# Kernel optimization log

Measured on AMD Instinct MI355X. Metric: run time of the kernel, lower is better.

## Reference

```python
import jax, jax.numpy as jnp
import numpy as np

# Pangu-Weather EarthSpecificBlock, layer-1 config
WZ, WH, WW = 2, 6, 12          # window size (z, lat, lon)
Z, H, W = 8, 91, 180           # token grid after patch embedding
C = 192                        # token dim
HEADS = 6
B = 1
PAD_TOP, PAD_BOT = 2, 3        # lat 91 -> 96 (CustomPad3d, centered)
ZP, HP, WP = 8, 96, 180        # padded grid
NWB = (ZP // WZ) * (HP // WH)  # 64 bias windows (z*lat)
N = WZ * WH * WW               # 144 tokens per window


def earth_position_index():
    zi = np.arange(WZ); zj = -np.arange(WZ) * WZ
    hi = np.arange(WH); hj = -np.arange(WH) * WH
    w = np.arange(WW)
    c1 = np.stack(np.meshgrid(zi, hi, w, indexing='ij')).reshape(3, -1)
    c2 = np.stack(np.meshgrid(zj, hj, w, indexing='ij')).reshape(3, -1)
    coords = (c1[:, :, None] - c2[:, None, :]).transpose(1, 2, 0).astype(np.int64)
    coords[:, :, 2] += WW - 1
    coords[:, :, 1] *= 2 * WW - 1
    coords[:, :, 0] *= (2 * WW - 1) * WH * WH
    return coords.sum(-1)  # (N, N) int indices into bias table

POS_IDX = jnp.asarray(earth_position_index())


def layer_norm(x, w, b, eps=1e-5):
    mu = x.mean(-1, keepdims=True)
    var = ((x - mu) ** 2).mean(-1, keepdims=True)
    return (x - mu) * jax.lax.rsqrt(var + eps) * w + b


def setup_inputs() -> dict:
    key = jax.random.key(0)
    ks = jax.random.split(key, 8)
    f = lambda k, s: jax.random.normal(k, s, jnp.float32) * 0.02
    return {
        "x": jax.random.normal(ks[0], (B, Z * H * W, C), jnp.float32),
        "qkv_w": f(ks[1], (3 * C, C)),
        "qkv_b": jnp.zeros((3 * C,), jnp.float32),
        "proj_w": f(ks[2], (C, C)),
        "proj_b": jnp.zeros((C,), jnp.float32),
        "bias_table": f(ks[3], ((2 * WW - 1) * WH * WH * WZ * WZ, NWB, HEADS)),
        "norm1_w": jnp.ones((C,), jnp.float32),
        "norm1_b": jnp.zeros((C,), jnp.float32),
        "norm2_w": jnp.ones((C,), jnp.float32),
        "norm2_b": jnp.zeros((C,), jnp.float32),
        "mlp_w1": f(ks[4], (4 * C, C)),
        "mlp_b1": jnp.zeros((4 * C,), jnp.float32),
        "mlp_w2": f(ks[5], (C, 4 * C)),
        "mlp_b2": jnp.zeros((C,), jnp.float32),
        "roll": 0,
    }


def reference(x, qkv_w, qkv_b, proj_w, proj_b, bias_table,
              norm1_w, norm1_b, norm2_w, norm2_b,
              mlp_w1, mlp_b1, mlp_w2, mlp_b2, roll):
    shortcut = x  # (B, L, C)
    hd = C // HEADS
    scale = hd ** -0.5
    xs = x.reshape(B, Z, H, W, C)
    xs = jnp.pad(xs, ((0, 0), (0, 0), (PAD_TOP, PAD_BOT), (0, 0), (0, 0)))
    # window partition: (B, ZP, HP, WP, C) -> (nb, N, C), windows ordered (z, lat, lon)
    xw = xs.reshape(B, ZP // WZ, WZ, HP // WH, WH, WP // WW, WW, C)
    xw = xw.transpose(0, 1, 3, 5, 2, 4, 6, 7).reshape(-1, N, C)
    nb = xw.shape[0]  # B * 64 * 15 = 960
    qkv = (xw @ qkv_w.T + qkv_b).reshape(nb, N, 3, HEADS, hd).transpose(2, 0, 3, 1, 4)
    q, k, v = qkv[0] * scale, qkv[1], qkv[2]  # each (nb, HEADS, N, hd)
    att = jnp.einsum('bhnd,bhmd->bhnm', q, k)  # (nb, HEADS, N, N)
    # earth-specific bias gathered via position index
    bias = bias_table[POS_IDX]                 # (N, N, NWB, HEADS)
    bias = bias.transpose(2, 3, 0, 1)          # (NWB, HEADS, N, N)
    # nb = B * NWB * n_lon_windows, NWB is the leading window factor
    att = att.reshape(B, NWB, -1, HEADS, N, N) + bias[None, :, None]
    att = jax.nn.softmax(att, axis=-1).reshape(nb, HEADS, N, N)
    out = jnp.einsum('bhnm,bhmd->bnhd', att, v).reshape(nb, N, C)
    out = out @ proj_w.T + proj_b
    # window reverse + crop padding
    out = out.reshape(B, ZP // WZ, HP // WH, WP // WW, WZ, WH, WW, C)
    out = out.transpose(0, 1, 4, 2, 5, 3, 6, 7).reshape(B, ZP, HP, WP, C)
    out = out[:, :, PAD_TOP:HP - PAD_BOT, :, :].reshape(B, -1, C)
    # post-norm residual (Pangu): x = shortcut + norm1(attn); x = x + norm2(mlp(x))
    x1 = shortcut + layer_norm(out, norm1_w, norm1_b)
    h1 = jax.nn.gelu(x1 @ mlp_w1.T + mlp_b1, approximate=False)
    mlp_out = h1 @ mlp_w2.T + mlp_b2
    return x1 + layer_norm(mlp_out, norm2_w, norm2_b)
```

## Files before the change

kernel.cpp:

```cpp
#include <hip/hip_runtime.h>
#include <hip/hip_bf16.h>

typedef __hip_bfloat16 bf16;
#define DEVI __device__ __forceinline__

typedef __bf16 bf16x8 __attribute__((ext_vector_type(8)));
typedef __bf16 bf16x4 __attribute__((ext_vector_type(4)));
typedef float  f32x4  __attribute__((ext_vector_type(4)));

DEVI float bf2f(bf16 v) { return __bfloat162float(v); }
DEVI bf16 f2bf(float v) { return __float2bfloat16(v); }
DEVI float bfu2f(unsigned short u) { return __uint_as_float((unsigned)u << 16); }

DEVI unsigned short bfbits(float x) {
    bf16 h = __float2bfloat16(x);
    return *reinterpret_cast<unsigned short*>(&h);
}
DEVI unsigned int pack2(float x, float y) {
    return (unsigned int)bfbits(x) | ((unsigned int)bfbits(y) << 16);
}
DEVI bf16x8 pack8(float4 lo, float4 hi) {
    union { unsigned int u[4]; bf16x8 v; } z;
    z.u[0] = pack2(lo.x, lo.y); z.u[1] = pack2(lo.z, lo.w);
    z.u[2] = pack2(hi.x, hi.y); z.u[3] = pack2(hi.z, hi.w);
    return z.v;
}
DEVI bf16x8 ld8h(const bf16* p) {
    bf16x4 lo = *(const bf16x4*)p;
    bf16x4 hi = *(const bf16x4*)(p + 4);
    return __builtin_shufflevector(lo, hi, 0, 1, 2, 3, 4, 5, 6, 7);
}

__global__ __launch_bounds__(256) void prep_attn_w(
    const float* __restrict__ qkv_w, const float* __restrict__ qkv_b,
    bf16* __restrict__ qkv_wb, float* __restrict__ qkv_bb)
{
    const float scale = 0.17677669529663687f;
    int idx = blockIdx.x * 256 + threadIdx.x;
    if (idx < 110592) {
        int c = idx % 192, d = idx / 192;
        int h = d / 96, q2 = d - h * 96, seg = q2 >> 5, rr = q2 & 31;
        float v = qkv_w[(size_t)(seg * 192 + h * 32 + rr) * 192 + c];
        if (seg == 0) v *= scale;
        qkv_wb[idx] = f2bf(v);
    }
    if (idx < 576) {
        int h = idx / 96, q2 = idx - h * 96, seg = q2 >> 5, rr = q2 & 31;
        float b = qkv_b[seg * 192 + h * 32 + rr];
        if (seg == 0) b *= scale;
        qkv_bb[idx] = b;
    }
}

__global__ __launch_bounds__(256) void prep_bias(
    const float* __restrict__ bias_table, bf16* __restrict__ biasT)
{
    int idx = blockIdx.x * 256 + threadIdx.x;
    if (idx >= 7962624) return;
    int m = idx % 144;
    int n = (idx / 144) % 144;
    int r2 = idx / 20736;
    int h = r2 % 6, wb = r2 / 6;
    int tzn = n / 72, thn = (n / 12) % 6, twn = n % 12;
    int tzm = m / 72, thm = (m / 12) % 6, twm = m % 12;
    int bidx = (tzn + 2 * tzm) * 828 + (thn + 6 * thm) * 23 + (twn - twm + 11);
    biasT[idx] = f2bf(bias_table[(size_t)(bidx * 64 + wb) * 6 + h]);
}

__global__ __launch_bounds__(256) void zero_vtpad(bf16* __restrict__ vt)
{
    int idx = blockIdx.x * 256 + threadIdx.x;
    if (idx >= 368640) return;
    int row = idx >> 1, half = idx & 1;
    uint4 z = make_uint4(0u, 0u, 0u, 0u);
    *(uint4*)(vt + (size_t)row * 160 + 144 + half * 8) = z;
}

__global__ __launch_bounds__(256, 2) void qkv_gemm_kernel(
    const float* __restrict__ x, const bf16* __restrict__ qkv_wb,
    const float* __restrict__ qkv_bb, bf16* __restrict__ qk,
    bf16* __restrict__ vt)
{
    __shared__ alignas(16) bf16 Xs[48 * 200];
    const int tid  = threadIdx.x;
    const int wave = tid >> 6;
    const int lane = tid & 63;
    const int quad = lane >> 4;
    const int l15  = lane & 15;
    const int b    = blockIdx.x;
    const int wi   = b / 3, tblk = b % 3;
    const int ww_  = wi % 15;
    const int hw   = (wi / 15) % 16;
    const int zw   = wi / 240;

    for (int i = tid; i < 48 * 24; i += 256) {
        int r = i / 24, c8 = i - r * 24;
        int t  = tblk * 48 + r;
        int tz = t / 72, rr = t - tz * 72;
        int th = rr / 12, tw = rr - th * 12;
        int lat = hw * 6 + th - 2;
        bool valid = (lat >= 0 && lat < 91);
        uint4 val = make_uint4(0u, 0u, 0u, 0u);
        if (valid) {
            size_t base = ((size_t)((zw * 2 + tz) * 91 + lat) * 180
                           + ww_ * 12 + tw) * 192;
            float4 lo = *(const float4*)(x + base + c8 * 8);
            float4 hi = *(const float4*)(x + base + c8 * 8 + 4);
            bf16x8 p = pack8(lo, hi);
            val = *(uint4*)&p;
        }
        *(uint4*)(Xs + r * 200 + c8 * 8) = val;
    }
    __syncthreads();

    bf16x8 af[3][6];
#pragma unroll
    for (int mt = 0; mt < 3; ++mt)
#pragma unroll
        for (int ks = 0; ks < 6; ++ks)
            af[mt][ks] = *(const bf16x8*)(Xs + (mt * 16 + l15) * 200 + ks * 32 + quad * 8);

    const int colw = wave * 144;
    for (int nt = 0; nt < 9; ++nt) {
        int c0  = colw + nt * 16;
        int h   = c0 / 96, q20 = c0 % 96;
        int seg = q20 >> 5, rr0 = q20 & 31;
        const bf16* wrow = qkv_wb + (size_t)(h * 96 + q20 + l15) * 192;
        bf16x8 wfr[6];
#pragma unroll
        for (int ks = 0; ks < 6; ++ks)
            wfr[ks] = *(const bf16x8*)(wrow + ks * 32 + quad * 8);
        float bias = qkv_bb[h * 96 + q20 + l15];

        f32x4 acc[3];
#pragma unroll
        for (int mt = 0; mt < 3; ++mt) acc[mt] = (f32x4){0.f, 0.f, 0.f, 0.f};
#pragma unroll
        for (int ks = 0; ks < 6; ++ks)
#pragma unroll
            for (int mt = 0; mt < 3; ++mt)
                acc[mt] = __builtin_amdgcn_mfma_f32_16x16x32_bf16(
                    af[mt][ks], wfr[ks], acc[mt], 0, 0, 0);

        if (seg < 2) {
            bf16* dst = qk + (size_t)((wi * 6 + h) * 2 + seg) * 4608 + rr0 + l15;
#pragma unroll
            for (int mt = 0; mt < 3; ++mt)
#pragma unroll
                for (int r = 0; r < 4; ++r) {
                    int tok = tblk * 48 + mt * 16 + quad * 4 + r;
                    dst[tok * 32] = f2bf(acc[mt][r] + bias);
                }
        } else {
            bf16* dst = vt + ((size_t)(wi * 6 + h) * 32 + rr0 + l15) * 160;
#pragma unroll
            for (int mt = 0; mt < 3; ++mt)
#pragma unroll
                for (int r = 0; r < 4; ++r) {
                    int tok = tblk * 48 + mt * 16 + quad * 4 + r;
                    dst[tok] = f2bf(acc[mt][r] + bias);
                }
        }
    }
}

__global__ __launch_bounds__(256, 4) void attn_slim_kernel(
    const bf16* __restrict__ qk, const bf16* __restrict__ vt,
    const bf16* __restrict__ biasT, bf16* __restrict__ attn_out)
{
    const int tid  = threadIdx.x;
    const int wave = tid >> 6;
    const int lane = tid & 63;
    const int quad = lane >> 4;
    const int l15  = lane & 15;

    const int bid     = blockIdx.x;
    const int logical = (bid & 7) * 720 + (bid >> 3);
    const int wi      = logical / 6;
    const int head    = logical % 6;
    const int hw = (wi / 15) % 16;
    const int zw = wi / 240;
    const int wb = zw * 16 + hw;

    const bf16* Qg = qk + (size_t)((wi * 6 + head) * 2) * 4608;
    const bf16* Kg = Qg + 4608;
    const bf16* Vg = vt + (size_t)(wi * 6 + head) * 32 * 160;
    const bf16* bt = biasT + (size_t)(wb * 6 + head) * 20736;

    for (int i = 0; i < 3; ++i) {
        int nti = wave + 4 * i;
        if (nti >= 9) continue;

        bf16x8 qb = *(const bf16x8*)(Qg + (nti * 16 + l15) * 32 + quad * 8);

        f32x4 st[9];
#pragma unroll
        for (int mt = 0; mt < 9; ++mt) {
            bf16x8 ka = *(const bf16x8*)(Kg + (mt * 16 + l15) * 32 + quad * 8);
            st[mt] = (f32x4){0.f, 0.f, 0.f, 0.f};
            st[mt] = __builtin_amdgcn_mfma_f32_16x16x32_bf16(
                ka, qb, st[mt], 0, 0, 0);
        }

        const bf16* brow = bt + (size_t)(nti * 16 + l15) * 144 + quad * 4;
#pragma unroll
        for (int mt = 0; mt < 9; ++mt) {
            union { bf16x4 v; unsigned short u[4]; } bb_;
            bb_.v = *(const bf16x4*)(brow + mt * 16);
#pragma unroll
            for (int r = 0; r < 4; ++r)
                st[mt][r] += bfu2f(bb_.u[r]);
        }

        float mx = -1e30f;
#pragma unroll
        for (int mt = 0; mt < 9; ++mt)
#pragma unroll
            for (int r = 0; r < 4; ++r) mx = fmaxf(mx, st[mt][r]);
        mx = fmaxf(mx, __shfl_xor(mx, 16, 64));
        mx = fmaxf(mx, __shfl_xor(mx, 32, 64));
        float s = 0.f;
#pragma unroll
        for (int mt = 0; mt < 9; ++mt)
#pragma unroll
            for (int r = 0; r < 4; ++r) {
                float e = __expf(st[mt][r] - mx);
                st[mt][r] = e;
                s += e;
            }
        s += __shfl_xor(s, 16, 64);
        s += __shfl_xor(s, 32, 64);
        float inv = 1.f / s;
#pragma unroll
        for (int mt = 0; mt < 9; ++mt)
#pragma unroll
            for (int r = 0; r < 4; ++r) st[mt][r] *= inv;

        f32x4 oa[2];
        oa[0] = (f32x4){0.f, 0.f, 0.f, 0.f};
        oa[1] = (f32x4){0.f, 0.f, 0.f, 0.f};
#pragma unroll
        for (int ks = 0; ks < 5; ++ks) {
            unsigned A0 = pack2(st[2 * ks][0], st[2 * ks][1]);
            unsigned A1 = pack2(st[2 * ks][2], st[2 * ks][3]);
            unsigned B0 = 0u, B1 = 0u;
            if (ks < 4) {
                B0 = pack2(st[2 * ks + 1][0], st[2 * ks + 1][1]);
                B1 = pack2(st[2 * ks + 1][2], st[2 * ks + 1][3]);
            }
            bool lo2 = quad < 2;
            unsigned Z0 = lo2 ? A0 : B0, Z1 = lo2 ? A1 : B1;
            unsigned Y0 = lo2 ? B0 : A0, Y1 = lo2 ? B1 : A1;
            unsigned s16_0 = __shfl_xor((int)Z0, 16, 64);
            unsigned s16_1 = __shfl_xor((int)Z1, 16, 64);
            unsigned s32_0 = __shfl_xor((int)Y0, 32, 64);
            unsigned s32_1 = __shfl_xor((int)Y1, 32, 64);
            unsigned s48_0 = __shfl_xor((int)Y0, 48, 64);
            unsigned s48_1 = __shfl_xor((int)Y1, 48, 64);
            union { unsigned u[4]; bf16x8 v; } fr;
            fr.u[0] = (quad == 0) ? Z0 : (quad == 1) ? s48_0 : (quad == 2) ? s32_0 : s16_0;
            fr.u[1] = (quad == 0) ? Z1 : (quad == 1) ? s48_1 : (quad == 2) ? s32_1 : s16_1;
            fr.u[2] = (quad == 0) ? s16_0 : (quad == 1) ? s32_0 : (quad == 2) ? s48_0 : Z0;
            fr.u[3] = (quad == 0) ? s16_1 : (quad == 1) ? s32_1 : (quad == 2) ? s48_1 : Z1;
#pragma unroll
            for (int n2 = 0; n2 < 2; ++n2) {
                bf16x8 vb = *(const bf16x8*)(Vg + (n2 * 16 + l15) * 160
                                             + ks * 32 + quad * 8);
                oa[n2] = __builtin_amdgcn_mfma_f32_16x16x32_bf16(
                    fr.v, vb, oa[n2], 0, 0, 0);
            }
        }

#pragma unroll
        for (int n2 = 0; n2 < 2; ++n2)
#pragma unroll
            for (int r = 0; r < 4; ++r) {
                int tok = nti * 16 + quad * 4 + r;
                attn_out[(size_t)(wi * 144 + tok) * 192 + (head << 5) + n2 * 16 + l15]
                    = f2bf(oa[n2][r]);
            }
    }
}

__global__ __launch_bounds__(256, 4) void attn_fused_kernel(
    const float* __restrict__ x, const bf16* __restrict__ qkv_wb,
    const float* __restrict__ qkv_bb, const bf16* __restrict__ biasT,
    bf16* __restrict__ attn_out)
{
    __shared__ alignas(16) char sm[30976];
    bf16* Qs  = (bf16*)sm;
    bf16* Ks  = (bf16*)(sm + 10368);
    bf16* VTs = (bf16*)(sm + 20736);

    const int tid  = threadIdx.x;
    const int wave = tid >> 6;
    const int lane = tid & 63;
    const int quad = lane >> 4;
    const int l15  = lane & 15;

    const int bid     = blockIdx.x;
    const int logical = (bid & 7) * 720 + (bid >> 3);
    const int wi      = logical / 6;
    const int head    = logical % 6;
    const int ww_  = wi % 15;
    const int hw   = (wi / 15) % 16;
    const int zw   = wi / 240;
    const int wb   = zw * 16 + hw;

    for (int i = tid; i < 512; i += 256) {
        int d = i >> 4, c = i & 15;
        VTs[d * 160 + 144 + c] = f2bf(0.f);
    }

    for (int i = 0; i < 3; ++i) {
        int mt = wave + 4 * i;
        if (mt < 9) {
            int t  = mt * 16 + l15;
            int tz = t / 72, rr = t - tz * 72;
            int th = rr / 12, tw = rr - th * 12;
            int lat = hw * 6 + th - 2;
            bool valid = (lat >= 0 && lat < 91);
            size_t base = ((size_t)((zw * 2 + tz) * 91 + (valid ? lat : 0)) * 180
                           + ww_ * 12 + tw) * 192;
            bf16x8 af[6];
#pragma unroll
            for (int ks = 0; ks < 6; ++ks) {
                float4 lo = make_float4(0.f, 0.f, 0.f, 0.f);
                float4 hi = make_float4(0.f, 0.f, 0.f, 0.f);
                if (valid) {
                    lo = *(const float4*)(x + base + ks * 32 + quad * 8);
                    hi = *(const float4*)(x + base + ks * 32 + quad * 8 + 4);
                }
                af[ks] = pack8(lo, hi);
            }
            for (int nt = 0; nt < 6; ++nt) {
                const bf16* wrow = qkv_wb + (size_t)(head * 96 + nt * 16 + l15) * 192;
                bf16x8 bw[6];
#pragma unroll
                for (int ks = 0; ks < 6; ++ks)
                    bw[ks] = *(const bf16x8*)(wrow + ks * 32 + quad * 8);
                float bias = qkv_bb[head * 96 + nt * 16 + l15];

                f32x4 acc = (f32x4){0.f, 0.f, 0.f, 0.f};
#pragma unroll
                for (int ks = 0; ks < 6; ++ks)
                    acc = __builtin_amdgcn_mfma_f32_16x16x32_bf16(
                        af[ks], bw[ks], acc, 0, 0, 0);
#pragma unroll
                for (int r = 0; r < 4; ++r) {
                    float v = acc[r] + bias;
                    int tok = mt * 16 + quad * 4 + r;
                    if (nt < 2)      Qs[tok * 36 + nt * 16 + l15] = f2bf(v);
                    else if (nt < 4) Ks[tok * 36 + (nt - 2) * 16 + l15] = f2bf(v);
                    else             VTs[((nt - 4) * 16 + l15) * 160 + tok] = f2bf(v);
                }
            }
        }
    }
    __syncthreads();

    const bf16* bt = biasT + (size_t)(wb * 6 + head) * 20736;

    for (int i = 0; i < 3; ++i) {
        int nti = wave + 4 * i;
        if (nti >= 9) continue;

        bf16x8 qb = ld8h(Qs + (nti * 16 + l15) * 36 + quad * 8);

        f32x4 st[9];
#pragma unroll
        for (int mt = 0; mt < 9; ++mt) {
            bf16x8 ka = ld8h(Ks + (mt * 16 + l15) * 36 + quad * 8);
            st[mt] = (f32x4){0.f, 0.f, 0.f, 0.f};
            st[mt] = __builtin_amdgcn_mfma_f32_16x16x32_bf16(
                ka, qb, st[mt], 0, 0, 0);
        }

        const bf16* brow = bt + (size_t)(nti * 16 + l15) * 144 + quad * 4;
#pragma unroll
        for (int mt = 0; mt < 9; ++mt) {
            union { bf16x4 v; unsigned short u[4]; } bb_;
            bb_.v = *(const bf16x4*)(brow + mt * 16);
#pragma unroll
            for (int r = 0; r < 4; ++r)
                st[mt][r] += bfu2f(bb_.u[r]);
        }

        float mx = -1e30f;
#pragma unroll
        for (int mt = 0; mt < 9; ++mt)
#pragma unroll
            for (int r = 0; r < 4; ++r) mx = fmaxf(mx, st[mt][r]);
        mx = fmaxf(mx, __shfl_xor(mx, 16, 64));
        mx = fmaxf(mx, __shfl_xor(mx, 32, 64));
        float s = 0.f;
#pragma unroll
        for (int mt = 0; mt < 9; ++mt)
#pragma unroll
            for (int r = 0; r < 4; ++r) {
                float e = __expf(st[mt][r] - mx);
                st[mt][r] = e;
                s += e;
            }
        s += __shfl_xor(s, 16, 64);
        s += __shfl_xor(s, 32, 64);
        float inv = 1.f / s;
#pragma unroll
        for (int mt = 0; mt < 9; ++mt)
#pragma unroll
            for (int r = 0; r < 4; ++r) st[mt][r] *= inv;

        f32x4 oa[2];
        oa[0] = (f32x4){0.f, 0.f, 0.f, 0.f};
        oa[1] = (f32x4){0.f, 0.f, 0.f, 0.f};
#pragma unroll
        for (int ks = 0; ks < 5; ++ks) {
            unsigned A0 = pack2(st[2 * ks][0], st[2 * ks][1]);
            unsigned A1 = pack2(st[2 * ks][2], st[2 * ks][3]);
            unsigned B0 = 0u, B1 = 0u;
            if (ks < 4) {
                B0 = pack2(st[2 * ks + 1][0], st[2 * ks + 1][1]);
                B1 = pack2(st[2 * ks + 1][2], st[2 * ks + 1][3]);
            }
            bool lo2 = quad < 2;
            unsigned Z0 = lo2 ? A0 : B0, Z1 = lo2 ? A1 : B1;
            unsigned Y0 = lo2 ? B0 : A0, Y1 = lo2 ? B1 : A1;
            unsigned s16_0 = __shfl_xor((int)Z0, 16, 64);
            unsigned s16_1 = __shfl_xor((int)Z1, 16, 64);
            unsigned s32_0 = __shfl_xor((int)Y0, 32, 64);
            unsigned s32_1 = __shfl_xor((int)Y1, 32, 64);
            unsigned s48_0 = __shfl_xor((int)Y0, 48, 64);
            unsigned s48_1 = __shfl_xor((int)Y1, 48, 64);
            union { unsigned u[4]; bf16x8 v; } fr;
            fr.u[0] = (quad == 0) ? Z0 : (quad == 1) ? s48_0 : (quad == 2) ? s32_0 : s16_0;
            fr.u[1] = (quad == 0) ? Z1 : (quad == 1) ? s48_1 : (quad == 2) ? s32_1 : s16_1;
            fr.u[2] = (quad == 0) ? s16_0 : (quad == 1) ? s32_0 : (quad == 2) ? s48_0 : Z0;
            fr.u[3] = (quad == 0) ? s16_1 : (quad == 1) ? s32_1 : (quad == 2) ? s48_1 : Z1;
#pragma unroll
            for (int n2 = 0; n2 < 2; ++n2) {
                bf16x8 vb = *(const bf16x8*)(VTs + (n2 * 16 + l15) * 160
                                             + ks * 32 + quad * 8);
                oa[n2] = __builtin_amdgcn_mfma_f32_16x16x32_bf16(
                    fr.v, vb, oa[n2], 0, 0, 0);
            }
        }

#pragma unroll
        for (int n2 = 0; n2 < 2; ++n2)
#pragma unroll
            for (int r = 0; r < 4; ++r) {
                int tok = nti * 16 + quad * 4 + r;
                attn_out[(size_t)(wi * 144 + tok) * 192 + (head << 5) + n2 * 16 + l15]
                    = f2bf(oa[n2][r]);
            }
    }
}

__global__ __launch_bounds__(256, 2) void proj_mfma_kernel(
    const bf16* __restrict__ attn, const float* __restrict__ proj_w,
    const float* __restrict__ proj_b, const float* __restrict__ xin,
    const float* __restrict__ n1w, const float* __restrict__ n1b,
    bf16* __restrict__ x1out)
{
    __shared__ alignas(16) char sm[56320];
    bf16*  Xs     = (bf16*)sm;
    float* wsum   = (float*)(sm + 51200);
    float* wsq    = (float*)(sm + 53248);
    float* mean_s = (float*)(sm + 55296);
    float* rstd_s = (float*)(sm + 55808);

    const int tid  = threadIdx.x;
    const int wave = tid >> 6;
    const int lane = tid & 63;
    const int quad = lane >> 4;
    const int l15  = lane & 15;
    const long tok0 = (long)blockIdx.x * 128;
    const int colw = wave * 48;

    for (int i = tid; i < 128 * 24; i += 256) {
        int r = i / 24, c4 = i - r * 24;
        long l = tok0 + r;
        uint4 v = make_uint4(0u, 0u, 0u, 0u);
        if (l < 131040) {
            int li  = (int)l;
            int z   = li / 16380, rem = li - z * 16380;
            int lat = rem / 180, lon = rem - lat * 180;
            int latp = lat + 2;
            int zw = z >> 1, tz = z & 1;
            int hw = latp / 6, th = latp - hw * 6;
            int wwn = lon / 12, tw = lon - wwn * 12;
            int wi = (zw * 16 + hw) * 15 + wwn;
            int t  = (tz * 6 + th) * 12 + tw;
            v = *(const uint4*)(attn + (size_t)(wi * 144 + t) * 192 + c4 * 8);
        }
        *(uint4*)(Xs + r * 200 + c4 * 8) = v;
    }
    __syncthreads();

    f32x4 o[3][8];
#pragma unroll
    for (int nt = 0; nt < 3; ++nt)
#pragma unroll
        for (int mt = 0; mt < 8; ++mt)
            o[nt][mt] = (f32x4){0.f, 0.f, 0.f, 0.f};

#pragma unroll
    for (int ks = 0; ks < 6; ++ks) {
        bf16x8 wfr[3];
#pragma unroll
        for (int nt = 0; nt < 3; ++nt) {
            const float* wp = proj_w + (size_t)(colw + nt * 16 + l15) * 192
                            + ks * 32 + quad * 8;
            float4 lo = *(const float4*)wp;
            float4 hi = *(const float4*)(wp + 4);
            wfr[nt] = pack8(lo, hi);
        }
#pragma unroll
        for (int mt = 0; mt < 8; ++mt) {
            bf16x8 a = *(const bf16x8*)(Xs + (mt * 16 + l15) * 200 + ks * 32 + quad * 8);
#pragma unroll
            for (int nt = 0; nt < 3; ++nt)
                o[nt][mt] = __builtin_amdgcn_mfma_f32_16x16x32_bf16(
                    a, wfr[nt], o[nt][mt], 0, 0, 0);
        }
    }

    float pbv[3], gw[3], gb[3];
#pragma unroll
    for (int nt = 0; nt < 3; ++nt) {
        int c = colw + nt * 16 + l15;
        pbv[nt] = proj_b[c];
        gw[nt]  = n1w[c];
        gb[nt]  = n1b[c];
    }
#pragma unroll
    for (int nt = 0; nt < 3; ++nt)
#pragma unroll
        for (int mt = 0; mt < 8; ++mt)
#pragma unroll
            for (int r = 0; r < 4; ++r)
                o[nt][mt][r] += pbv[nt];

#pragma unroll
    for (int mt = 0; mt < 8; ++mt) {
#pragma unroll
        for (int r = 0; r < 4; ++r) {
            float p = o[0][mt][r] + o[1][mt][r] + o[2][mt][r];
            float q = o[0][mt][r] * o[0][mt][r] + o[1][mt][r] * o[1][mt][r]
                    + o[2][mt][r] * o[2][mt][r];
#pragma unroll
            for (int m_ = 1; m_ < 16; m_ <<= 1) {
                p += __shfl_xor(p, m_, 64);
                q += __shfl_xor(q, m_, 64);
            }
            if (l15 == 0) {
                int row = mt * 16 + quad * 4 + r;
                wsum[row * 4 + wave] = p;
                wsq [row * 4 + wave] = q;
            }
        }
    }
    __syncthreads();
    if (tid < 128) {
        float s  = wsum[tid * 4] + wsum[tid * 4 + 1] + wsum[tid * 4 + 2] + wsum[tid * 4 + 3];
        float ss = wsq [tid * 4] + wsq [tid * 4 + 1] + wsq [tid * 4 + 2] + wsq [tid * 4 + 3];
        float m = s * (1.f / 192.f);
        float var = ss * (1.f / 192.f) - m * m;
        mean_s[tid] = m;
        rstd_s[tid] = rsqrtf(fmaxf(var, 0.f) + 1e-5f);
    }
    __syncthreads();

#pragma unroll
    for (int mt = 0; mt < 8; ++mt) {
#pragma unroll
        for (int r = 0; r < 4; ++r) {
            int row = mt * 16 + quad * 4 + r;
            long tok = tok0 + row;
            if (tok < 131040) {
                float m = mean_s[row], rsd = rstd_s[row];
#pragma unroll
                for (int nt = 0; nt < 3; ++nt) {
                    int c = colw + nt * 16 + l15;
                    float val = (o[nt][mt][r] - m) * rsd * gw[nt] + gb[nt]
                              + xin[(size_t)tok * 192 + c];
                    x1out[(size_t)tok * 192 + c] = f2bf(val);
                }
            }
        }
    }
}

__global__ __launch_bounds__(256) void prep_weights(
    const float* __restrict__ w1, const float* __restrict__ w2,
    unsigned int* __restrict__ w1b, unsigned int* __restrict__ w2b)
{
    int i = blockIdx.x * 256 + threadIdx.x;
    if (i < 73728) {
        w1b[i] = pack2(w1[2 * i], w1[2 * i + 1]);
    } else {
        int j = i - 73728;
        w2b[j] = pack2(w2[2 * j], w2[2 * j + 1]);
    }
}

__global__ __launch_bounds__(256, 2) void mlp_mfma_kernel(
    const bf16* __restrict__ x1, const bf16* __restrict__ w1b,
    const float* __restrict__ b1, const bf16* __restrict__ w2b,
    const float* __restrict__ b2, const float* __restrict__ n2w,
    const float* __restrict__ n2b, float* __restrict__ out)
{
    __shared__ alignas(16) char sm[28160];
    bf16*  Bs     = (bf16*)sm;
    float* wsum   = (float*)(sm + 25600);
    float* wsq    = (float*)(sm + 26624);
    float* mean_s = (float*)(sm + 27648);
    float* rstd_s = (float*)(sm + 27904);

    const int tid  = threadIdx.x;
    const int wave = tid >> 6;
    const int lane = tid & 63;
    const int quad = lane >> 4;
    const int l15  = lane & 15;
    const long tok0 = (long)blockIdx.x * 64;
    const int colw = wave * 48;

    for (int i = tid; i < 64 * 24; i += 256) {
        int r = i / 24, c8 = i - r * 24;
        uint4 v = make_uint4(0u, 0u, 0u, 0u);
        if (tok0 + r < 131040)
            v = *(const uint4*)(x1 + (tok0 + r) * 192 + (size_t)c8 * 8);
        *(uint4*)(Bs + r * 200 + c8 * 8) = v;
    }
    __syncthreads();

    bf16x8 af[4][6];
#pragma unroll
    for (int mt = 0; mt < 4; ++mt)
#pragma unroll
        for (int ks = 0; ks < 6; ++ks)
            af[mt][ks] = *(const bf16x8*)(Bs + (mt * 16 + l15) * 200 + ks * 32 + quad * 8);

    f32x4 o[3][4];
#pragma unroll
    for (int nt = 0; nt < 3; ++nt)
#pragma unroll
        for (int mt = 0; mt < 4; ++mt)
            o[nt][mt] = (f32x4){0.f, 0.f, 0.f, 0.f};

    for (int nc = 0; nc < 4; ++nc) {
        f32x4 g[3][4];
#pragma unroll
        for (int nt = 0; nt < 3; ++nt)
#pragma unroll
            for (int mt = 0; mt < 4; ++mt)
                g[nt][mt] = (f32x4){0.f, 0.f, 0.f, 0.f};
        const int h0 = nc * 192 + colw;
#pragma unroll
        for (int ks = 0; ks < 6; ++ks) {
            bf16x8 bfr[3];
#pragma unroll
            for (int nt = 0; nt < 3; ++nt)
                bfr[nt] = *(const bf16x8*)(w1b + (size_t)(h0 + nt * 16 + l15) * 192 + ks * 32 + quad * 8);
#pragma unroll
            for (int nt = 0; nt < 3; ++nt)
#pragma unroll
                for (int mt = 0; mt < 4; ++mt)
                    g[nt][mt] = __builtin_amdgcn_mfma_f32_16x16x32_bf16(
                        af[mt][ks], bfr[nt], g[nt][mt], 0, 0, 0);
        }
        __syncthreads();

#pragma unroll
        for (int nt = 0; nt < 3; ++nt) {
            float bb = b1[h0 + nt * 16 + l15];
            int hcol = colw + nt * 16 + l15;
#pragma unroll
            for (int mt = 0; mt < 4; ++mt) {
#pragma unroll
                for (int r = 0; r < 4; ++r) {
                    float v = g[nt][mt][r] + bb;
                    float w = v * (1.5957691216057308f + 0.07135481627025f * v * v);
                    float e = __expf(w);
                    float gl = v - v / (e + 1.f);
                    Bs[(mt * 16 + quad * 4 + r) * 200 + hcol] = f2bf(gl);
                }
            }
        }
        __syncthreads();

#pragma unroll
        for (int ks = 0; ks < 6; ++ks) {
            bf16x8 hf[4];
#pragma unroll
            for (int mt = 0; mt < 4; ++mt)
                hf[mt] = *(const bf16x8*)(Bs + (mt * 16 + l15) * 200 + ks * 32 + quad * 8);
            bf16x8 wf[3];
#pragma unroll
            for (int nt = 0; nt < 3; ++nt)
                wf[nt] = *(const bf16x8*)(w2b + (size_t)(colw + nt * 16 + l15) * 768 + nc * 192 + ks * 32 + quad * 8);
#pragma unroll
            for (int nt = 0; nt < 3; ++nt)
#pragma unroll
                for (int mt = 0; mt < 4; ++mt)
                    o[nt][mt] = __builtin_amdgcn_mfma_f32_16x16x32_bf16(
                        hf[mt], wf[nt], o[nt][mt], 0, 0, 0);
        }
    }

    float b2v[3], gw[3], gb[3];
#pragma unroll
    for (int nt = 0; nt < 3; ++nt) {
        int c = colw + nt * 16 + l15;
        b2v[nt] = b2[c];
        gw[nt] = n2w[c];
        gb[nt] = n2b[c];
    }
#pragma unroll
    for (int nt = 0; nt < 3; ++nt)
#pragma unroll
        for (int mt = 0; mt < 4; ++mt)
#pragma unroll
            for (int r = 0; r < 4; ++r)
                o[nt][mt][r] += b2v[nt];

#pragma unroll
    for (int mt = 0; mt < 4; ++mt) {
#pragma unroll
        for (int r = 0; r < 4; ++r) {
            float p = o[0][mt][r] + o[1][mt][r] + o[2][mt][r];
            float q = o[0][mt][r] * o[0][mt][r] + o[1][mt][r] * o[1][mt][r]
                    + o[2][mt][r] * o[2][mt][r];
#pragma unroll
            for (int m_ = 1; m_ < 16; m_ <<= 1) {
                p += __shfl_xor(p, m_, 64);
                q += __shfl_xor(q, m_, 64);
            }
            if (l15 == 0) {
                int row = mt * 16 + quad * 4 + r;
                wsum[row * 4 + wave] = p;
                wsq [row * 4 + wave] = q;
            }
        }
    }
    __syncthreads();
    if (tid < 64) {
        float s  = wsum[tid * 4] + wsum[tid * 4 + 1] + wsum[tid * 4 + 2] + wsum[tid * 4 + 3];
        float ss = wsq [tid * 4] + wsq [tid * 4 + 1] + wsq [tid * 4 + 2] + wsq [tid * 4 + 3];
        float m = s * (1.f / 192.f);
        float var = ss * (1.f / 192.f) - m * m;
        mean_s[tid] = m;
        rstd_s[tid] = rsqrtf(fmaxf(var, 0.f) + 1e-5f);
    }
    __syncthreads();

#pragma unroll
    for (int mt = 0; mt < 4; ++mt) {
#pragma unroll
        for (int r = 0; r < 4; ++r) {
            int row = mt * 16 + quad * 4 + r;
            long tok = tok0 + row;
            if (tok < 131040) {
                float m = mean_s[row], rsd = rstd_s[row];
#pragma unroll
                for (int nt = 0; nt < 3; ++nt) {
                    int c = colw + nt * 16 + l15;
                    float val = (o[nt][mt][r] - m) * rsd * gw[nt] + gb[nt]
                              + bf2f(x1[(size_t)tok * 192 + c]);
                    out[tok * 192 + c] = val;
                }
            }
        }
    }
}

extern "C" void kernel_launch(void* const* d_in, const int* in_sizes, int n_in,
                              void* d_out, int out_size, void* d_ws, size_t ws_size,
                              hipStream_t stream) {
    (void)in_sizes; (void)n_in; (void)out_size;
    const float* x          = (const float*)d_in[0];
    const float* qkv_w      = (const float*)d_in[1];
    const float* qkv_b      = (const float*)d_in[2];
    const float* proj_w     = (const float*)d_in[3];
    const float* proj_b     = (const float*)d_in[4];
    const float* bias_table = (const float*)d_in[5];
    const float* n1w        = (const float*)d_in[6];
    const float* n1b        = (const float*)d_in[7];
    const float* n2w        = (const float*)d_in[8];
    const float* n2b        = (const float*)d_in[9];
    const float* w1         = (const float*)d_in[10];
    const float* b1         = (const float*)d_in[11];
    const float* w2         = (const float*)d_in[12];
    const float* b2         = (const float*)d_in[13];
    float* out = (float*)d_out;

    const size_t SPLIT_WS = 234383616ULL;
    if (ws_size >= SPLIT_WS) {
        bf16*  attn_ws = (bf16*)d_ws;
        bf16*  qkg     = (bf16*)((char*)d_ws + 53084160);
        bf16*  vtg     = (bf16*)((char*)d_ws + 159252480);
        bf16*  biasT   = (bf16*)((char*)d_ws + 218234880);
        bf16*  qkv_wb  = (bf16*)((char*)d_ws + 234160128);
        float* qkv_bb  = (float*)((char*)d_ws + 234381312);
        bf16*  x1_ws   = (bf16*)((char*)d_ws + 53084160);
        bf16*  w1b     = (bf16*)((char*)d_ws + 103403520);
        bf16*  w2b     = (bf16*)((char*)d_ws + 103698432);

        prep_attn_w<<<432, 256, 0, stream>>>(qkv_w, qkv_b, qkv_wb, qkv_bb);
        prep_bias<<<31104, 256, 0, stream>>>(bias_table, biasT);
        zero_vtpad<<<1440, 256, 0, stream>>>(vtg);
        qkv_gemm_kernel<<<2880, 256, 0, stream>>>(x, qkv_wb, qkv_bb, qkg, vtg);
        attn_slim_kernel<<<5760, 256, 0, stream>>>(qkg, vtg, biasT, attn_ws);
        proj_mfma_kernel<<<1024, 256, 0, stream>>>(attn_ws, proj_w, proj_b, x, n1w, n1b, x1_ws);
        prep_weights<<<576, 256, 0, stream>>>(w1, w2, (unsigned int*)w1b, (unsigned int*)w2b);
        mlp_mfma_kernel<<<2048, 256, 0, stream>>>(x1_ws, w1b, b1, w2b, b2, n2w, n2b, out);
    } else {
        bf16*  attn_ws = (bf16*)d_ws;
        bf16*  x1_ws   = (bf16*)((char*)d_ws + 53084160);
        bf16*  w1b     = (bf16*)d_ws;
        bf16*  w2b     = (bf16*)((char*)d_ws + 294912);
        bf16*  qkv_wb  = (bf16*)((char*)d_ws + 53084160);
        float* qkv_bb  = (float*)((char*)d_ws + 53305344);
        bf16*  biasT   = (bf16*)((char*)d_ws + 53307648);

        prep_attn_w<<<432, 256, 0, stream>>>(qkv_w, qkv_b, qkv_wb, qkv_bb);
        prep_bias<<<31104, 256, 0, stream>>>(bias_table, biasT);
        attn_fused_kernel<<<5760, 256, 0, stream>>>(x, qkv_wb, qkv_bb, biasT, attn_ws);
        proj_mfma_kernel<<<1024, 256, 0, stream>>>(attn_ws, proj_w, proj_b, x, n1w, n1b, x1_ws);
        prep_weights<<<576, 256, 0, stream>>>(w1, w2, (unsigned int*)w1b, (unsigned int*)w2b);
        mlp_mfma_kernel<<<2048, 256, 0, stream>>>(x1_ws, w1b, b1, w2b, b2, n2w, n2b, out);
    }
}
```

Measured before the change: 720.7 us.

## Restructure MLP kernel so each wave owns 16 tokens with register-only hidden activations

The MLP kernel now assigns each wave 16 tokens and all 192 output columns, computing the hidden layer transposed (W1·x) in 32-column chunks. GELU outputs are reshuffled across lanes with shuffles into the A-operand layout for the second GEMM, so shared memory and the block barriers go away. LayerNorm statistics reduce within the wave only. The trade-off is that weight reuse across waves is lost, since each wave streams all of W1 and W2 for just 16 tokens. It also raises register pressure through 12 accumulators.

```diff
diff --git a/kernel.cpp b/kernel.cpp
--- a/kernel.cpp
+++ b/kernel.cpp
@@ -610,165 +610,120 @@
     const float* __restrict__ b2, const float* __restrict__ n2w,
     const float* __restrict__ n2b, float* __restrict__ out)
 {
-    __shared__ alignas(16) char sm[28160];
-    bf16*  Bs     = (bf16*)sm;
-    float* wsum   = (float*)(sm + 25600);
-    float* wsq    = (float*)(sm + 26624);
-    float* mean_s = (float*)(sm + 27648);
-    float* rstd_s = (float*)(sm + 27904);
-
     const int tid  = threadIdx.x;
     const int wave = tid >> 6;
     const int lane = tid & 63;
     const int quad = lane >> 4;
     const int l15  = lane & 15;
-    const long tok0 = (long)blockIdx.x * 64;
-    const int colw = wave * 48;
-
-    for (int i = tid; i < 64 * 24; i += 256) {
-        int r = i / 24, c8 = i - r * 24;
-        uint4 v = make_uint4(0u, 0u, 0u, 0u);
-        if (tok0 + r < 131040)
-            v = *(const uint4*)(x1 + (tok0 + r) * 192 + (size_t)c8 * 8);
-        *(uint4*)(Bs + r * 200 + c8 * 8) = v;
-    }
-    __syncthreads();
-
-    bf16x8 af[4][6];
-#pragma unroll
-    for (int mt = 0; mt < 4; ++mt)
-#pragma unroll
-        for (int ks = 0; ks < 6; ++ks)
-            af[mt][ks] = *(const bf16x8*)(Bs + (mt * 16 + l15) * 200 + ks * 32 + quad * 8);
-
-    f32x4 o[3][4];
-#pragma unroll
-    for (int nt = 0; nt < 3; ++nt)
-#pragma unroll
-        for (int mt = 0; mt < 4; ++mt)
-            o[nt][mt] = (f32x4){0.f, 0.f, 0.f, 0.f};
-
-    for (int nc = 0; nc < 4; ++nc) {
-        f32x4 g[3][4];
-#pragma unroll
-        for (int nt = 0; nt < 3; ++nt)
-#pragma unroll
-            for (int mt = 0; mt < 4; ++mt)
-                g[nt][mt] = (f32x4){0.f, 0.f, 0.f, 0.f};
-        const int h0 = nc * 192 + colw;
+    const long tok0 = (long)blockIdx.x * 64 + wave * 16;
+
+    const long mytok = tok0 + l15;
+    const bool tv = (mytok < 131040);
+    bf16x8 af[6];
+#pragma unroll
+    for (int ks = 0; ks < 6; ++ks) {
+        if (tv)
+            af[ks] = *(const bf16x8*)(x1 + (size_t)mytok * 192 + ks * 32 + quad * 8);
+        else {
+            union { unsigned u[4]; bf16x8 v; } z; z.u[0] = z.u[1] = z.u[2] = z.u[3] = 0u;
+            af[ks] = z.v;
+        }
+    }
+
+    f32x4 o[12];
+#pragma unroll
+    for (int ct = 0; ct < 12; ++ct) o[ct] = (f32x4){0.f, 0.f, 0.f, 0.f};
+
+    for (int c = 0; c < 24; ++c) {
+        const int h0 = c * 32;
+        f32x4 gA = (f32x4){0.f, 0.f, 0.f, 0.f};
+        f32x4 gB = (f32x4){0.f, 0.f, 0.f, 0.f};
 #pragma unroll
         for (int ks = 0; ks < 6; ++ks) {
-            bf16x8 bfr[3];
-#pragma unroll
-            for (int nt = 0; nt < 3; ++nt)
-                bfr[nt] = *(const bf16x8*)(w1b + (size_t)(h0 + nt * 16 + l15) * 192 + ks * 32 + quad * 8);
-#pragma unroll
-            for (int nt = 0; nt < 3; ++nt)
-#pragma unroll
-                for (int mt = 0; mt < 4; ++mt)
-                    g[nt][mt] = __builtin_amdgcn_mfma_f32_16x16x32_bf16(
-                        af[mt][ks], bfr[nt], g[nt][mt], 0, 0, 0);
-        }
-        __syncthreads();
-
-#pragma unroll
-        for (int nt = 0; nt < 3; ++nt) {
-            float bb = b1[h0 + nt * 16 + l15];
-            int hcol = colw + nt * 16 + l15;
-#pragma unroll
-            for (int mt = 0; mt < 4; ++mt) {
-#pragma unroll
-                for (int r = 0; r < 4; ++r) {
-                    float v = g[nt][mt][r] + bb;
-                    float w = v * (1.5957691216057308f + 0.07135481627025f * v * v);
-                    float e = __expf(w);
-                    float gl = v - v / (e + 1.f);
-                    Bs[(mt * 16 + quad * 4 + r) * 200 + hcol] = f2bf(gl);
-                }
-            }
-        }
-        __syncthreads();
-
-#pragma unroll
-        for (int ks = 0; ks < 6; ++ks) {
-            bf16x8 hf[4];
-#pragma unroll
-            for (int mt = 0; mt < 4; ++mt)
-                hf[mt] = *(const bf16x8*)(Bs + (mt * 16 + l15) * 200 + ks * 32 + quad * 8);
-            bf16x8 wf[3];
-#pragma unroll
-            for (int nt = 0; nt < 3; ++nt)
-                wf[nt] = *(const bf16x8*)(w2b + (size_t)(colw + nt * 16 + l15) * 768 + nc * 192 + ks * 32 + quad * 8);
-#pragma unroll
-            for (int nt = 0; nt < 3; ++nt)
-#pragma unroll
-                for (int mt = 0; mt < 4; ++mt)
-                    o[nt][mt] = __builtin_amdgcn_mfma_f32_16x16x32_bf16(
-                        hf[mt], wf[nt], o[nt][mt], 0, 0, 0);
-        }
-    }
-
-    float b2v[3], gw[3], gb[3];
-#pragma unroll
-    for (int nt = 0; nt < 3; ++nt) {
-        int c = colw + nt * 16 + l15;
-        b2v[nt] = b2[c];
-        gw[nt] = n2w[c];
-        gb[nt] = n2b[c];
-    }
-#pragma unroll
-    for (int nt = 0; nt < 3; ++nt)
-#pragma unroll
-        for (int mt = 0; mt < 4; ++mt)
-#pragma unroll
-            for (int r = 0; r < 4; ++r)
-                o[nt][mt][r] += b2v[nt];
-
-#pragma unroll
-    for (int mt = 0; mt < 4; ++mt) {
+            bf16x8 wA = *(const bf16x8*)(w1b + (size_t)(h0 + l15) * 192 + ks * 32 + quad * 8);
+            bf16x8 wB = *(const bf16x8*)(w1b + (size_t)(h0 + 16 + l15) * 192 + ks * 32 + quad * 8);
+            gA = __builtin_amdgcn_mfma_f32_16x16x32_bf16(wA, af[ks], gA, 0, 0, 0);
+            gB = __builtin_amdgcn_mfma_f32_16x16x32_bf16(wB, af[ks], gB, 0, 0, 0);
+        }
+        float4 bA = *(const float4*)(b1 + h0 + quad * 4);
+        float4 bB = *(const float4*)(b1 + h0 + 16 + quad * 4);
 #pragma unroll
         for (int r = 0; r < 4; ++r) {
-            float p = o[0][mt][r] + o[1][mt][r] + o[2][mt][r];
-            float q = o[0][mt][r] * o[0][mt][r] + o[1][mt][r] * o[1][mt][r]
-                    + o[2][mt][r] * o[2][mt][r];
-#pragma unroll
-            for (int m_ = 1; m_ < 16; m_ <<= 1) {
-                p += __shfl_xor(p, m_, 64);
-                q += __shfl_xor(q, m_, 64);
-            }
-            if (l15 == 0) {
-                int row = mt * 16 + quad * 4 + r;
-                wsum[row * 4 + wave] = p;
-                wsq [row * 4 + wave] = q;
-            }
-        }
-    }
-    __syncthreads();
-    if (tid < 64) {
-        float s  = wsum[tid * 4] + wsum[tid * 4 + 1] + wsum[tid * 4 + 2] + wsum[tid * 4 + 3];
-        float ss = wsq [tid * 4] + wsq [tid * 4 + 1] + wsq [tid * 4 + 2] + wsq [tid * 4 + 3];
-        float m = s * (1.f / 192.f);
-        float var = ss * (1.f / 192.f) - m * m;
-        mean_s[tid] = m;
-        rstd_s[tid] = rsqrtf(fmaxf(var, 0.f) + 1e-5f);
-    }
-    __syncthreads();
-
-#pragma unroll
-    for (int mt = 0; mt < 4; ++mt) {
-#pragma unroll
-        for (int r = 0; r < 4; ++r) {
-            int row = mt * 16 + quad * 4 + r;
-            long tok = tok0 + row;
-            if (tok < 131040) {
-                float m = mean_s[row], rsd = rstd_s[row];
-#pragma unroll
-                for (int nt = 0; nt < 3; ++nt) {
-                    int c = colw + nt * 16 + l15;
-                    float val = (o[nt][mt][r] - m) * rsd * gw[nt] + gb[nt]
-                              + bf2f(x1[(size_t)tok * 192 + c]);
-                    out[tok * 192 + c] = val;
-                }
+            float vA = gA[r] + ((const float*)&bA)[r];
+            float wA_ = vA * (1.5957691216057308f + 0.07135481627025f * vA * vA);
+            gA[r] = vA - vA / (__expf(wA_) + 1.f);
+            float vB = gB[r] + ((const float*)&bB)[r];
+            float wB_ = vB * (1.5957691216057308f + 0.07135481627025f * vB * vB);
+            gB[r] = vB - vB / (__expf(wB_) + 1.f);
+        }
+        unsigned A0 = pack2(gA[0], gA[1]);
+        unsigned A1 = pack2(gA[2], gA[3]);
+        unsigned B0 = pack2(gB[0], gB[1]);
+        unsigned B1 = pack2(gB[2], gB[3]);
+        bool lo2 = quad < 2;
+        unsigned Z0 = lo2 ? A0 : B0, Z1 = lo2 ? A1 : B1;
+        unsigned Y0 = lo2 ? B0 : A0, Y1 = lo2 ? B1 : A1;
+        unsigned s16_0 = __shfl_xor((int)Z0, 16, 64);
+        unsigned s16_1 = __shfl_xor((int)Z1, 16, 64);
+        unsigned s32_0 = __shfl_xor((int)Y0, 32, 64);
+        unsigned s32_1 = __shfl_xor((int)Y1, 32, 64);
+        unsigned s48_0 = __shfl_xor((int)Y0, 48, 64);
+        unsigned s48_1 = __shfl_xor((int)Y1, 48, 64);
+        union { unsigned u[4]; bf16x8 v; } fr;
+        fr.u[0] = (quad == 0) ? Z0 : (quad == 1) ? s48_0 : (quad == 2) ? s32_0 : s16_0;
+        fr.u[1] = (quad == 0) ? Z1 : (quad == 1) ? s48_1 : (quad == 2) ? s32_1 : s16_1;
+        fr.u[2] = (quad == 0) ? s16_0 : (quad == 1) ? s32_0 : (quad == 2) ? s48_0 : Z0;
+        fr.u[3] = (quad == 0) ? s16_1 : (quad == 1) ? s32_1 : (quad == 2) ? s48_1 : Z1;
+#pragma unroll
+        for (int ct = 0; ct < 12; ++ct) {
+            bf16x8 wf = *(const bf16x8*)(w2b + (size_t)(ct * 16 + l15) * 768 + h0 + quad * 8);
+            o[ct] = __builtin_amdgcn_mfma_f32_16x16x32_bf16(fr.v, wf, o[ct], 0, 0, 0);
+        }
+    }
+
+    float b2v[12], gw[12], gb[12];
+#pragma unroll
+    for (int ct = 0; ct < 12; ++ct) {
+        int cc = ct * 16 + l15;
+        b2v[ct] = b2[cc];
+        gw[ct]  = n2w[cc];
+        gb[ct]  = n2b[cc];
+    }
+#pragma unroll
+    for (int ct = 0; ct < 12; ++ct)
+#pragma unroll
+        for (int r = 0; r < 4; ++r) o[ct][r] += b2v[ct];
+
+    float mean_r[4], rstd_r[4];
+#pragma unroll
+    for (int r = 0; r < 4; ++r) {
+        float p = 0.f, q = 0.f;
+#pragma unroll
+        for (int ct = 0; ct < 12; ++ct) {
+            p += o[ct][r];
+            q += o[ct][r] * o[ct][r];
+        }
+#pragma unroll
+        for (int m_ = 1; m_ < 16; m_ <<= 1) {
+            p += __shfl_xor(p, m_, 64);
+            q += __shfl_xor(q, m_, 64);
+        }
+        float m = p * (1.f / 192.f);
+        float var = q * (1.f / 192.f) - m * m;
+        mean_r[r] = m;
+        rstd_r[r] = rsqrtf(fmaxf(var, 0.f) + 1e-5f);
+    }
+
+#pragma unroll
+    for (int r = 0; r < 4; ++r) {
+        long tok = tok0 + quad * 4 + r;
+        if (tok < 131040) {
+#pragma unroll
+            for (int ct = 0; ct < 12; ++ct) {
+                int cc = ct * 16 + l15;
+                float val = (o[ct][r] - mean_r[r]) * rstd_r[r] * gw[ct] + gb[ct]
+                          + bf2f(x1[(size_t)tok * 192 + cc]);
+                out[tok * 192 + cc] = val;
             }
         }
     }
```

Result: slower. 1.122 ms (+55.6%).
